# Optimization experiments

Hardware: AMD Instinct MI355X
Metric: run time of the kernel (lower is better)

The kernel has to match this reference:

```python
import jax, jax.numpy as jnp
from jax import lax
import numpy as np

PATCH_H = 8
PATCH_W = 8


def setup_inputs() -> dict:
    key = jax.random.key(0)
    k1, k2 = jax.random.split(key)
    x = jax.random.normal(k1, (2, 1024, 256, 256), dtype=jnp.float32)
    # Conv1d weight [C_out, C_in, k], bias=False
    conv_w = jax.random.normal(k2, (1024, 1024, 3), dtype=jnp.float32) * 0.02
    return {"x": x, "conv_w": conv_w}


def reference(x, conv_w):
    B, C, H, W = x.shape
    hf, wf = H // PATCH_H, W // PATCH_W
    P = hf * wf
    # Patch average pool: mean over each (PATCH_H, PATCH_W) tile -> [B, C, hf, wf]
    xp = x.reshape(B, C, hf, PATCH_H, wf, PATCH_W)
    y = xp.mean(axis=(3, 5)).reshape(B, C, P)
    # Conv1d over the patch axis (SAME padding, no bias), then sigmoid gate
    g = lax.conv_general_dilated(
        y, conv_w, window_strides=(1,), padding="SAME",
        dimension_numbers=("NCH", "OIH", "NCH"))
    g = jax.nn.sigmoid(g).reshape(B, C, hf, wf)
    # Broadcast gate back over each patch and multiply
    out = xp * g[:, :, :, None, :, None]
    return out.reshape(B, C, H, W)
```

## Files before the change

### kernel.cpp

```cpp
#include <hip/hip_runtime.h>
#include <hip/hip_bf16.h>

#define HH 256
#define WW 256
#define CCH 1024
#define PP 1024

using f32x4 = __attribute__((ext_vector_type(4))) float;
using short8 = __attribute__((ext_vector_type(8))) short;

__device__ __forceinline__ void pool_direct_body(const float* __restrict__ xb,
                                                 __hip_bfloat16* __restrict__ yTb,
                                                 int job, int t) {
    __shared__ float lds[32][33];
    int ph = job >> 5, c0 = (job & 31) * 32;
    int wid = t >> 6, lane = t & 63;
#pragma unroll 2
    for (int i = 0; i < 8; ++i) {
        int cl = wid * 8 + i;
        const float* base = xb + (size_t)(c0 + cl) * (HH * WW)
                          + (size_t)ph * 8 * WW + lane * 4;
        float acc = 0.f;
#pragma unroll
        for (int r = 0; r < 8; ++r) {
            f32x4 v = __builtin_nontemporal_load((const f32x4*)(base + r * WW));
            acc += v.x + v.y + v.z + v.w;
        }
        acc += __shfl_xor(acc, 1);
        if ((lane & 1) == 0)
            lds[lane >> 1][cl] = acc * (1.f / 64.f);
    }
    __syncthreads();
    if (t < 128) {
        int row = t >> 2, q = t & 3;
        short8 s;
#pragma unroll
        for (int j = 0; j < 8; ++j) {
            __hip_bfloat16 h = __float2bfloat16(lds[row][q * 8 + j]);
            s[j] = (short)reinterpret_cast<unsigned short&>(h);
        }
        *(short8*)(yTb + (size_t)(1 + ph * 32 + row) * CCH + c0 + q * 8) = s;
    }
}

__device__ __forceinline__ void gemm_body(const __hip_bfloat16* __restrict__ wT,
                                          const __hip_bfloat16* __restrict__ yTb,
                                          float* __restrict__ gateb,
                                          int job, int tid) {
    int lane = tid & 63;
    int wid  = tid >> 6;
    int l15 = lane & 15, lhi = lane >> 4;
    int co_base = (job & 15) * 64 + wid * 16;
    int p_base  = (job >> 4) * 32;
    f32x4 acc[2] = {};
#pragma unroll
    for (int tap = 0; tap < 3; ++tap) {
        const __hip_bfloat16* Ap = wT + (size_t)tap * (1u << 20)
                                 + (size_t)(co_base + l15) * CCH + lhi * 8;
        const __hip_bfloat16* Bp = yTb + (size_t)(p_base + l15 + tap) * CCH + lhi * 8;
        for (int ci0 = 0; ci0 < CCH; ci0 += 32) {
            short8 a0 = *(const short8*)(Ap + ci0);
            short8 b0 = *(const short8*)(Bp + ci0);
            short8 b1 = *(const short8*)(Bp + ci0 + 16 * CCH);
            acc[0] = __builtin_amdgcn_mfma_f32_16x16x32_bf16(a0, b0, acc[0], 0, 0, 0);
            acc[1] = __builtin_amdgcn_mfma_f32_16x16x32_bf16(a0, b1, acc[1], 0, 0, 0);
        }
    }
#pragma unroll
    for (int j16 = 0; j16 < 2; ++j16) {
        int col  = p_base + j16 * 16 + l15;
        int row0 = co_base + lhi * 4;
#pragma unroll
        for (int r = 0; r < 4; ++r)
            gateb[(size_t)(row0 + r) * PP + col] = 1.f / (1.f + __expf(-acc[j16][r]));
    }
}

__device__ __forceinline__ void apply_body(const float* __restrict__ xb,
                                           const float* __restrict__ gateb,
                                           float* __restrict__ outb,
                                           int c, int t) {
    __shared__ __align__(16) float g[PP];
    const float* xp = xb   + (size_t)c * (HH * WW);
    float*       op = outb + (size_t)c * (HH * WW);
    ((f32x4*)g)[t] = ((const f32x4*)(gateb + (size_t)c * PP))[t];
    __syncthreads();
    int col4 = t & 63;
    int r    = t >> 6;
    int pc   = col4 >> 1;
#pragma unroll 4
    for (int it = 0; it < 64; ++it) {
        int row = it * 4 + r;
        float gg = g[(row >> 3) * 32 + pc];
        size_t off = (size_t)row * 64 + col4;
        f32x4 v = __builtin_nontemporal_load((const f32x4*)xp + off);
        v *= gg;
        __builtin_nontemporal_store(v, (f32x4*)op + off);
    }
}

__global__ __launch_bounds__(256) void pool0_wconv_kernel(
        const float* __restrict__ x, const float* __restrict__ w,
        __hip_bfloat16* __restrict__ yT, __hip_bfloat16* __restrict__ wT) {
    int bid = blockIdx.x, t = threadIdx.x;
    if (bid < 1024) {
        pool_direct_body(x, yT, bid, t);
    } else {
        int base = (bid - 1024) * 256 + t;
#pragma unroll
        for (int it = 0; it < 16; ++it) {
            int idx = it * (1 << 16) + base;
            const float* p = w + (size_t)idx * 3;
            wT[idx]               = __float2bfloat16(p[0]);
            wT[(1u << 20) + idx]  = __float2bfloat16(p[1]);
            wT[(2u << 20) + idx]  = __float2bfloat16(p[2]);
        }
        if (base < 2 * CCH) {
            int bb = base >> 10, cc = base & 1023;
            __hip_bfloat16 z = __float2bfloat16(0.f);
            __hip_bfloat16* basep = yT + (size_t)bb * (PP + 2) * CCH;
            basep[cc] = z;
            basep[(size_t)(PP + 1) * CCH + cc] = z;
        }
    }
}

__global__ __launch_bounds__(256) void gemm0_pool1_kernel(
        const float* __restrict__ x, const __hip_bfloat16* __restrict__ wT,
        __hip_bfloat16* __restrict__ yT, float* __restrict__ gate) {
    int bid = blockIdx.x, t = threadIdx.x;
    if (bid < 512) {
        gemm_body(wT, yT, gate, bid, t);
    } else {
        const float* x1 = x + (size_t)CCH * HH * WW;
        __hip_bfloat16* yT1 = yT + (size_t)(PP + 2) * CCH;
        pool_direct_body(x1, yT1, bid - 512, t);
    }
}

__global__ __launch_bounds__(256) void gemm1_apply0_kernel(
        const float* __restrict__ x, const __hip_bfloat16* __restrict__ wT,
        const __hip_bfloat16* __restrict__ yT, float* __restrict__ gate,
        float* __restrict__ out) {
    int bid = blockIdx.x, t = threadIdx.x;
    if (bid < 512) {
        const __hip_bfloat16* yT1 = yT + (size_t)(PP + 2) * CCH;
        float* gate1 = gate + (size_t)CCH * PP;
        gemm_body(wT, yT1, gate1, bid, t);
    } else {
        apply_body(x, gate, out, 1023 - (bid - 512), t);
    }
}

__global__ __launch_bounds__(256) void apply1_kernel(
        const float* __restrict__ x, const float* __restrict__ gate,
        float* __restrict__ out) {
    const float* x1    = x    + (size_t)CCH * HH * WW;
    const float* gate1 = gate + (size_t)CCH * PP;
    float*       out1  = out  + (size_t)CCH * HH * WW;
    apply_body(x1, gate1, out1, 1023 - blockIdx.x, threadIdx.x);
}

extern "C" void kernel_launch(void* const* d_in, const int* in_sizes, int n_in,
                              void* d_out, int out_size, void* d_ws, size_t ws_size,
                              hipStream_t stream) {
    const float* x = (const float*)d_in[0];
    const float* w = (const float*)d_in[1];
    float* out = (float*)d_out;

    char* ws = (char*)d_ws;
    __hip_bfloat16* yT   = (__hip_bfloat16*)(ws);
    __hip_bfloat16* wT   = (__hip_bfloat16*)(ws + 4202496);
    float*          gate = (float*)(ws + 10493952);

    hipLaunchKernelGGL(pool0_wconv_kernel, dim3(1280), dim3(256), 0, stream,
                       x, w, yT, wT);
    hipLaunchKernelGGL(gemm0_pool1_kernel, dim3(1536), dim3(256), 0, stream,
                       x, wT, yT, gate);
    hipLaunchKernelGGL(gemm1_apply0_kernel, dim3(1536), dim3(256), 0, stream,
                       x, wT, yT, gate, out);
    hipLaunchKernelGGL(apply1_kernel, dim3(1024), dim3(256), 0, stream,
                       x, gate, out);
}
```

Measured before the change: 404.4 us.

## Split pool/gemm/apply into four spatial stripes and software-pipeline across ten launches

Splits each batch's 256 rows into four 64-row stripes and builds a nine-phase schedule. Each launch runs the GEMM for one stripe, the pool for a later stripe and the apply for an earlier stripe, so the MFMA work overlaps with memory-bound pooling and gating. Stripes are sized so the x data just pooled may still be in cache when it is re-read for the apply step. The pool and apply loads also drop their nontemporal hints to allow that cache reuse. In exchange it adds more kernel launches and smaller GEMM grids of 128 blocks, which can leave the device underused.

```diff
diff --git a/kernel.cpp b/kernel.cpp
--- a/kernel.cpp
+++ b/kernel.cpp
@@ -5,13 +5,15 @@
 #define WW 256
 #define CCH 1024
 #define PP 1024
+#define SROWS 64
+#define SPATCH 256
 
 using f32x4 = __attribute__((ext_vector_type(4))) float;
 using short8 = __attribute__((ext_vector_type(8))) short;
 
-__device__ __forceinline__ void pool_direct_body(const float* __restrict__ xb,
-                                                 __hip_bfloat16* __restrict__ yTb,
-                                                 int job, int t) {
+__device__ __forceinline__ void pool_body(const float* __restrict__ xb,
+                                          __hip_bfloat16* __restrict__ yTb,
+                                          int job, int t) {
     __shared__ float lds[32][33];
     int ph = job >> 5, c0 = (job & 31) * 32;
     int wid = t >> 6, lane = t & 63;
@@ -23,7 +25,7 @@
         float acc = 0.f;
 #pragma unroll
         for (int r = 0; r < 8; ++r) {
-            f32x4 v = __builtin_nontemporal_load((const f32x4*)(base + r * WW));
+            f32x4 v = *(const f32x4*)(base + r * WW);
             acc += v.x + v.y + v.z + v.w;
         }
         acc += __shfl_xor(acc, 1);
@@ -46,12 +48,12 @@
 __device__ __forceinline__ void gemm_body(const __hip_bfloat16* __restrict__ wT,
                                           const __hip_bfloat16* __restrict__ yTb,
                                           float* __restrict__ gateb,
-                                          int job, int tid) {
+                                          int s, int job, int tid) {
     int lane = tid & 63;
     int wid  = tid >> 6;
     int l15 = lane & 15, lhi = lane >> 4;
     int co_base = (job & 15) * 64 + wid * 16;
-    int p_base  = (job >> 4) * 32;
+    int p_base  = s * SPATCH + (job >> 4) * 32;
     f32x4 acc[2] = {};
 #pragma unroll
     for (int tap = 0; tap < 3; ++tap) {
@@ -79,34 +81,33 @@
 __device__ __forceinline__ void apply_body(const float* __restrict__ xb,
                                            const float* __restrict__ gateb,
                                            float* __restrict__ outb,
-                                           int c, int t) {
-    __shared__ __align__(16) float g[PP];
-    const float* xp = xb   + (size_t)c * (HH * WW);
-    float*       op = outb + (size_t)c * (HH * WW);
-    ((f32x4*)g)[t] = ((const f32x4*)(gateb + (size_t)c * PP))[t];
+                                           int s, int plane, int t) {
+    __shared__ __align__(16) float g[SPATCH];
+    const float* xp = xb   + (size_t)plane * (HH * WW) + (size_t)s * SROWS * WW;
+    float*       op = outb + (size_t)plane * (HH * WW) + (size_t)s * SROWS * WW;
+    if (t < 64)
+        ((f32x4*)g)[t] = ((const f32x4*)(gateb + (size_t)plane * PP + s * SPATCH))[t];
     __syncthreads();
     int col4 = t & 63;
     int r    = t >> 6;
     int pc   = col4 >> 1;
 #pragma unroll 4
-    for (int it = 0; it < 64; ++it) {
+    for (int it = 0; it < 16; ++it) {
         int row = it * 4 + r;
         float gg = g[(row >> 3) * 32 + pc];
         size_t off = (size_t)row * 64 + col4;
-        f32x4 v = __builtin_nontemporal_load((const f32x4*)xp + off);
+        f32x4 v = *((const f32x4*)xp + off);
         v *= gg;
         __builtin_nontemporal_store(v, (f32x4*)op + off);
     }
 }
 
-__global__ __launch_bounds__(256) void pool0_wconv_kernel(
+__global__ __launch_bounds__(256) void phaseA_kernel(
         const float* __restrict__ x, const float* __restrict__ w,
         __hip_bfloat16* __restrict__ yT, __hip_bfloat16* __restrict__ wT) {
     int bid = blockIdx.x, t = threadIdx.x;
-    if (bid < 1024) {
-        pool_direct_body(x, yT, bid, t);
-    } else {
-        int base = (bid - 1024) * 256 + t;
+    if (bid < 256) {
+        int base = bid * 256 + t;
 #pragma unroll
         for (int it = 0; it < 16; ++it) {
             int idx = it * (1 << 16) + base;
@@ -122,43 +123,41 @@
             basep[cc] = z;
             basep[(size_t)(PP + 1) * CCH + cc] = z;
         }
+    } else {
+        int s = (bid - 256) >> 8;
+        int job = (bid - 256) & 255;
+        pool_body(x, yT, s * SPATCH + job, t);
     }
 }
 
-__global__ __launch_bounds__(256) void gemm0_pool1_kernel(
-        const float* __restrict__ x, const __hip_bfloat16* __restrict__ wT,
-        __hip_bfloat16* __restrict__ yT, float* __restrict__ gate) {
+__global__ __launch_bounds__(256) void phase_kernel(
+        const float* __restrict__ x, float* __restrict__ out,
+        __hip_bfloat16* __restrict__ yT, __hip_bfloat16* __restrict__ wT,
+        float* __restrict__ gate,
+        int gB, int gS, int pB, int pS, int aB, int aS) {
     int bid = blockIdx.x, t = threadIdx.x;
-    if (bid < 512) {
-        gemm_body(wT, yT, gate, bid, t);
-    } else {
-        const float* x1 = x + (size_t)CCH * HH * WW;
-        __hip_bfloat16* yT1 = yT + (size_t)(PP + 2) * CCH;
-        pool_direct_body(x1, yT1, bid - 512, t);
+    int nG = (gB >= 0) ? 128 : 0;
+    int nP = (pB >= 0) ? 256 : 0;
+    if (bid < nG) {
+        const __hip_bfloat16* yTb = yT + (size_t)gB * (PP + 2) * CCH;
+        float* gateb = gate + (size_t)gB * CCH * PP;
+        gemm_body(wT, yTb, gateb, gS, bid, t);
+        return;
     }
-}
-
-__global__ __launch_bounds__(256) void gemm1_apply0_kernel(
-        const float* __restrict__ x, const __hip_bfloat16* __restrict__ wT,
-        const __hip_bfloat16* __restrict__ yT, float* __restrict__ gate,
-        float* __restrict__ out) {
-    int bid = blockIdx.x, t = threadIdx.x;
-    if (bid < 512) {
-        const __hip_bfloat16* yT1 = yT + (size_t)(PP + 2) * CCH;
-        float* gate1 = gate + (size_t)CCH * PP;
-        gemm_body(wT, yT1, gate1, bid, t);
-    } else {
-        apply_body(x, gate, out, 1023 - (bid - 512), t);
+    bid -= nG;
+    if (bid < nP) {
+        const float* xb = x + (size_t)pB * CCH * HH * WW;
+        __hip_bfloat16* yTb = yT + (size_t)pB * (PP + 2) * CCH;
+        pool_body(xb, yTb, pS * SPATCH + bid, t);
+        return;
     }
-}
-
-__global__ __launch_bounds__(256) void apply1_kernel(
-        const float* __restrict__ x, const float* __restrict__ gate,
-        float* __restrict__ out) {
-    const float* x1    = x    + (size_t)CCH * HH * WW;
-    const float* gate1 = gate + (size_t)CCH * PP;
-    float*       out1  = out  + (size_t)CCH * HH * WW;
-    apply_body(x1, gate1, out1, 1023 - blockIdx.x, threadIdx.x);
+    bid -= nP;
+    {
+        const float* xb = x + (size_t)aB * CCH * HH * WW;
+        const float* gateb = gate + (size_t)aB * CCH * PP;
+        float* outb = out + (size_t)aB * CCH * HH * WW;
+        apply_body(xb, gateb, outb, aS, bid, t);
+    }
 }
 
 extern "C" void kernel_launch(void* const* d_in, const int* in_sizes, int n_in,
@@ -173,12 +172,25 @@
     __hip_bfloat16* wT   = (__hip_bfloat16*)(ws + 4202496);
     float*          gate = (float*)(ws + 10493952);
 
-    hipLaunchKernelGGL(pool0_wconv_kernel, dim3(1280), dim3(256), 0, stream,
-                       x, w, yT, wT);
-    hipLaunchKernelGGL(gemm0_pool1_kernel, dim3(1536), dim3(256), 0, stream,
-                       x, wT, yT, gate);
-    hipLaunchKernelGGL(gemm1_apply0_kernel, dim3(1536), dim3(256), 0, stream,
-                       x, wT, yT, gate, out);
-    hipLaunchKernelGGL(apply1_kernel, dim3(1024), dim3(256), 0, stream,
-                       x, gate, out);
+    struct Ph { int gB, gS, pB, pS, aB, aS; };
+    const Ph phases[] = {
+        { 0, 0,  0, 2, -1, -1},
+        { 0, 1,  0, 3,  0,  0},
+        { 0, 2,  1, 0,  0,  1},
+        { 0, 3,  1, 1,  0,  2},
+        { 1, 0,  1, 2,  0,  3},
+        { 1, 1,  1, 3,  1,  0},
+        { 1, 2, -1, -1, 1,  1},
+        { 1, 3, -1, -1, 1,  2},
+        {-1, -1, -1, -1, 1, 3},
+    };
+
+    hipLaunchKernelGGL(phaseA_kernel, dim3(768), dim3(256), 0, stream, x, w, yT, wT);
+    for (const Ph& p : phases) {
+        int grid = (p.gB >= 0 ? 128 : 0) + (p.pB >= 0 ? 256 : 0)
+                 + (p.aB >= 0 ? 1024 : 0);
+        hipLaunchKernelGGL(phase_kernel, dim3(grid), dim3(256), 0, stream,
+                           x, out, yT, wT, gate,
+                           p.gB, p.gS, p.pB, p.pS, p.aB, p.aS);
+    }
 }
```

Result: slower. 447.3 us (+10.6%).
